# Kernel tuning notes

Measured on AMD Instinct MI355X. Metric: run time of the kernel, lower is better.

Reference implementation:

```python
import jax, jax.numpy as jnp
import numpy as np

NUM_INSTANCES = 64  # instance ids in [0, 64); id 0 is background and excluded


def _variance_smooth_loss(variances, ins_labels, num_segments):
    # variances: [N, D] float, ins_labels: [N] int
    N, D = variances.shape
    ones = jnp.ones((N,), dtype=variances.dtype)
    counts = jax.ops.segment_sum(ones, ins_labels, num_segments=num_segments)          # [S]
    sums = jax.ops.segment_sum(variances, ins_labels, num_segments=num_segments)       # [S, D]
    safe_counts = jnp.maximum(counts, 1.0)
    means = sums / safe_counts[:, None]                                                # per-instance mean [S, D]
    diff = variances - means[ins_labels]                                               # gather means back [N, D]
    sq = jnp.sum(diff * diff, axis=1)                                                  # [N]
    # per-instance MSE = sum of squared diffs / (K_i * D), matching nn.MSELoss (mean reduction)
    per_ins = jax.ops.segment_sum(sq, ins_labels, num_segments=num_segments) / (safe_counts * D)
    valid = (counts > 0) & (jnp.arange(num_segments) != 0)                             # skip id 0 & absent ids
    return jnp.sum(jnp.where(valid, per_ins, jnp.zeros_like(per_ins)))


def setup_inputs() -> dict:
    key = jax.random.key(0)
    k1, k2 = jax.random.split(key)
    N, D = 4_000_000, 8
    variances = jax.random.normal(k1, (N, D), dtype=jnp.float32)
    ins_labels = jax.random.randint(k2, (N,), 0, NUM_INSTANCES, dtype=jnp.int32)
    return {"variances": variances, "ins_labels": ins_labels}


def reference(variances, ins_labels):
    return _variance_smooth_loss(variances, ins_labels, NUM_INSTANCES)
```

## Files before the change

kernel.cpp:

```cpp
#include <hip/hip_runtime.h>

#define NUM_INST 64
#define BLOCK 256
#define GRID 3125
#define TILE_ROWS 256
#define SROW 9
#define PSTRIDE 1088
#define CHUNK 125

typedef __attribute__((ext_vector_type(8))) short bf16x8;
typedef __attribute__((ext_vector_type(4))) float f32x4;

__global__ __launch_bounds__(BLOCK) void vsl_main(const float4* __restrict__ rows,
                                                  const int* __restrict__ labels,
                                                  float* __restrict__ partial,
                                                  int n, int ntiles) {
    __shared__ float S[TILE_ROWS * SROW];
    __shared__ alignas(16) int Lab[TILE_ROWS];
    __shared__ float Cred[4][64];

    const int tid = threadIdx.x;
    const int w = tid >> 6;
    const int lane = tid & 63;
    const int g = lane >> 4;
    const int nn = lane & 15;
    const int f = nn & 7;
    const bool hi = nn >= 8;
    const int inst = 16 * w + nn;

    f32x4 acc = {0.f, 0.f, 0.f, 0.f};
    float cntf = 0.f;

    for (int tile = blockIdx.x; tile < ntiles; tile += GRID) {
        {
            const int r = 64 * w + lane;
            const int gr = tile * TILE_ROWS + r;
            const bool valid = gr < n;
            float4 a = make_float4(0, 0, 0, 0), b = make_float4(0, 0, 0, 0);
            int lb = 0;
            if (valid) { a = rows[2 * gr]; b = rows[2 * gr + 1]; lb = labels[gr]; }
            float* sp = &S[r * SROW];
            sp[0] = a.x; sp[1] = a.y; sp[2] = a.z; sp[3] = a.w;
            sp[4] = b.x; sp[5] = b.y; sp[6] = b.z; sp[7] = b.w;
            Lab[r] = lb;
            unsigned long long Md = __ballot(valid);
#pragma unroll
            for (int bp = 0; bp < 6; ++bp) {
                const unsigned long long bb = __ballot((lb >> bp) & 1);
                Md &= ((lane >> bp) & 1) ? bb : ~bb;
            }
            cntf += (float)__popcll(Md);
        }
        __syncthreads();

#pragma unroll
        for (int kb = 0; kb < 8; ++kb) {
            const int rb = kb * 32 + 8 * g;

            const float* bp0 = &S[rb * SROW + f];
            union { int i[4]; bf16x8 v; } bf;
#pragma unroll
            for (int jp = 0; jp < 4; ++jp) {
                float v0 = bp0[(2 * jp) * SROW];
                float v1 = bp0[(2 * jp + 1) * SROW];
                if (hi) { v0 *= v0; v1 *= v1; }
                const unsigned u0 = __float_as_uint(v0) + 0x8000u;
                const unsigned u1 = __float_as_uint(v1) + 0x8000u;
                bf.i[jp] = (int)__builtin_amdgcn_perm(u1, u0, 0x07060302u);
            }

            const int4 l0 = *(const int4*)&Lab[rb];
            const int4 l1 = *(const int4*)&Lab[rb + 4];
            union { int i[4]; bf16x8 v; } af;
            af.i[0] = ((l0.x == inst) ? 0x3F80 : 0) | ((l0.y == inst) ? 0x3F800000 : 0);
            af.i[1] = ((l0.z == inst) ? 0x3F80 : 0) | ((l0.w == inst) ? 0x3F800000 : 0);
            af.i[2] = ((l1.x == inst) ? 0x3F80 : 0) | ((l1.y == inst) ? 0x3F800000 : 0);
            af.i[3] = ((l1.z == inst) ? 0x3F80 : 0) | ((l1.w == inst) ? 0x3F800000 : 0);

            acc = __builtin_amdgcn_mfma_f32_16x16x32_bf16(af.v, bf.v, acc, 0, 0, 0);
        }
        __syncthreads();
    }

    Cred[w][lane] = cntf;
    __syncthreads();
    float* pb = &partial[(size_t)blockIdx.x * PSTRIDE];
#pragma unroll
    for (int r4 = 0; r4 < 4; ++r4) {
        const int instk = 16 * w + 4 * g + r4;
        pb[instk * 16 + nn] = acc[r4];
    }
    if (w == 0) {
        pb[1024 + lane] = Cred[0][lane] + Cred[1][lane] + Cred[2][lane] + Cred[3][lane];
    }
}

__global__ __launch_bounds__(BLOCK) void vsl_reduce(const float* __restrict__ partial,
                                                    float* __restrict__ gacc) {
    const int id = blockIdx.x * BLOCK + threadIdx.x;
    if (id >= 25 * PSTRIDE) return;
    const int chunk = id / PSTRIDE;
    const int j = id - chunk * PSTRIDE;
    float s = 0.f;
    const float* p = &partial[(size_t)chunk * CHUNK * PSTRIDE + j];
#pragma unroll 5
    for (int q = 0; q < CHUNK; ++q) s += p[(size_t)q * PSTRIDE];
    atomicAdd(&gacc[j], s);
}

__global__ __launch_bounds__(64) void vsl_final(const float* __restrict__ gacc,
                                                float* __restrict__ out) {
    const int i = threadIdx.x;
    float val = 0.f;
    const float cnt = gacc[1024 + i];
    if (i != 0 && cnt > 0.f) {
        const float* base = &gacc[i * 16];
        float ss = 0.f, m2 = 0.f;
#pragma unroll
        for (int d = 0; d < 8; ++d) {
            m2 += base[d] * base[d];
            ss += base[8 + d];
        }
        val = (ss - m2 / cnt) / (cnt * 8.0f);
    }
#pragma unroll
    for (int off = 32; off > 0; off >>= 1) val += __shfl_down(val, off, 64);
    if (i == 0) out[0] = val;
}

extern "C" void kernel_launch(void* const* d_in, const int* in_sizes, int n_in,
                              void* d_out, int out_size, void* d_ws, size_t ws_size,
                              hipStream_t stream) {
    const float* variances = (const float*)d_in[0];
    const int* labels = (const int*)d_in[1];
    const int n = in_sizes[1];
    const int ntiles = (n + TILE_ROWS - 1) / TILE_ROWS;

    float* gacc = (float*)d_ws;
    float* partial = (float*)((char*)d_ws + 8192);

    hipMemsetAsync(gacc, 0, PSTRIDE * sizeof(float), stream);
    vsl_main<<<GRID, BLOCK, 0, stream>>>((const float4*)variances, labels, partial, n, ntiles);
    vsl_reduce<<<(25 * PSTRIDE + BLOCK - 1) / BLOCK, BLOCK, 0, stream>>>(partial, gacc);
    vsl_final<<<1, 64, 0, stream>>>(gacc, (float*)d_out);
}
```

Measured before the change: 212.5 us.

## Pre-convert tiles to bf16 MFMA layout in LDS and prefetch next tile

Result: no change. 210.7 us (-0.9%).

```diff
diff --git a/kernel.cpp b/kernel.cpp
--- a/kernel.cpp
+++ b/kernel.cpp
@@ -4,7 +4,6 @@
 #define BLOCK 256
 #define GRID 3125
 #define TILE_ROWS 256
-#define SROW 9
 #define PSTRIDE 1088
 #define CHUNK 125
 
@@ -15,7 +14,7 @@
                                                   const int* __restrict__ labels,
                                                   float* __restrict__ partial,
                                                   int n, int ntiles) {
-    __shared__ float S[TILE_ROWS * SROW];
+    __shared__ alignas(16) short MT[8 * 16 * 4 * 8];
     __shared__ alignas(16) int Lab[TILE_ROWS];
     __shared__ float Cred[4][64];
 
@@ -24,51 +23,58 @@
     const int lane = tid & 63;
     const int g = lane >> 4;
     const int nn = lane & 15;
-    const int f = nn & 7;
-    const bool hi = nn >= 8;
     const int inst = 16 * w + nn;
+
+    const int r = tid;
+    const int wbase = ((r >> 5) * 512) + (((r >> 3) & 3) * 8) + (r & 7);
 
     f32x4 acc = {0.f, 0.f, 0.f, 0.f};
     float cntf = 0.f;
 
-    for (int tile = blockIdx.x; tile < ntiles; tile += GRID) {
-        {
-            const int r = 64 * w + lane;
-            const int gr = tile * TILE_ROWS + r;
-            const bool valid = gr < n;
-            float4 a = make_float4(0, 0, 0, 0), b = make_float4(0, 0, 0, 0);
-            int lb = 0;
-            if (valid) { a = rows[2 * gr]; b = rows[2 * gr + 1]; lb = labels[gr]; }
-            float* sp = &S[r * SROW];
-            sp[0] = a.x; sp[1] = a.y; sp[2] = a.z; sp[3] = a.w;
-            sp[4] = b.x; sp[5] = b.y; sp[6] = b.z; sp[7] = b.w;
-            Lab[r] = lb;
-            unsigned long long Md = __ballot(valid);
+    int tile = blockIdx.x;
+    bool pv = false;
+    float4 pa = make_float4(0, 0, 0, 0), pb = make_float4(0, 0, 0, 0);
+    int plb = 0;
+    if (tile < ntiles) {
+        const int gr = tile * TILE_ROWS + r;
+        pv = gr < n;
+        if (pv) { pa = rows[2 * gr]; pb = rows[2 * gr + 1]; plb = labels[gr]; }
+    }
+
+    while (tile < ntiles) {
+        unsigned long long Md = __ballot(pv);
 #pragma unroll
-            for (int bp = 0; bp < 6; ++bp) {
-                const unsigned long long bb = __ballot((lb >> bp) & 1);
-                Md &= ((lane >> bp) & 1) ? bb : ~bb;
-            }
-            cntf += (float)__popcll(Md);
+        for (int bp = 0; bp < 6; ++bp) {
+            const unsigned long long bb = __ballot((plb >> bp) & 1);
+            Md &= ((lane >> bp) & 1) ? bb : ~bb;
         }
+        cntf += (float)__popcll(Md);
+
+        float v[16];
+        v[0] = pa.x; v[1] = pa.y; v[2] = pa.z; v[3] = pa.w;
+        v[4] = pb.x; v[5] = pb.y; v[6] = pb.z; v[7] = pb.w;
+#pragma unroll
+        for (int c = 0; c < 8; ++c) v[8 + c] = v[c] * v[c];
+#pragma unroll
+        for (int c = 0; c < 16; ++c) {
+            const unsigned u = __float_as_uint(v[c]) + 0x8000u;
+            MT[wbase + c * 32] = (short)(u >> 16);
+        }
+        Lab[r] = plb;
         __syncthreads();
+
+        const int nt = tile + GRID;
+        pv = false; pa = make_float4(0, 0, 0, 0); pb = make_float4(0, 0, 0, 0); plb = 0;
+        if (nt < ntiles) {
+            const int gr = nt * TILE_ROWS + r;
+            pv = gr < n;
+            if (pv) { pa = rows[2 * gr]; pb = rows[2 * gr + 1]; plb = labels[gr]; }
+        }
 
 #pragma unroll
         for (int kb = 0; kb < 8; ++kb) {
             const int rb = kb * 32 + 8 * g;
-
-            const float* bp0 = &S[rb * SROW + f];
-            union { int i[4]; bf16x8 v; } bf;
-#pragma unroll
-            for (int jp = 0; jp < 4; ++jp) {
-                float v0 = bp0[(2 * jp) * SROW];
-                float v1 = bp0[(2 * jp + 1) * SROW];
-                if (hi) { v0 *= v0; v1 *= v1; }
-                const unsigned u0 = __float_as_uint(v0) + 0x8000u;
-                const unsigned u1 = __float_as_uint(v1) + 0x8000u;
-                bf.i[jp] = (int)__builtin_amdgcn_perm(u1, u0, 0x07060302u);
-            }
-
+            const bf16x8 bfrag = *(const bf16x8*)&MT[kb * 512 + nn * 32 + g * 8];
             const int4 l0 = *(const int4*)&Lab[rb];
             const int4 l1 = *(const int4*)&Lab[rb + 4];
             union { int i[4]; bf16x8 v; } af;
@@ -76,22 +82,22 @@
             af.i[1] = ((l0.z == inst) ? 0x3F80 : 0) | ((l0.w == inst) ? 0x3F800000 : 0);
             af.i[2] = ((l1.x == inst) ? 0x3F80 : 0) | ((l1.y == inst) ? 0x3F800000 : 0);
             af.i[3] = ((l1.z == inst) ? 0x3F80 : 0) | ((l1.w == inst) ? 0x3F800000 : 0);
-
-            acc = __builtin_amdgcn_mfma_f32_16x16x32_bf16(af.v, bf.v, acc, 0, 0, 0);
+            acc = __builtin_amdgcn_mfma_f32_16x16x32_bf16(af.v, bfrag, acc, 0, 0, 0);
         }
         __syncthreads();
+        tile = nt;
     }
 
     Cred[w][lane] = cntf;
     __syncthreads();
-    float* pb = &partial[(size_t)blockIdx.x * PSTRIDE];
+    float* pbk = &partial[(size_t)blockIdx.x * PSTRIDE];
 #pragma unroll
     for (int r4 = 0; r4 < 4; ++r4) {
         const int instk = 16 * w + 4 * g + r4;
-        pb[instk * 16 + nn] = acc[r4];
+        pbk[instk * 16 + nn] = acc[r4];
     }
     if (w == 0) {
-        pb[1024 + lane] = Cred[0][lane] + Cred[1][lane] + Cred[2][lane] + Cred[3][lane];
+        pbk[1024 + lane] = Cred[0][lane] + Cred[1][lane] + Cred[2][lane] + Cred[3][lane];
     }
 }
 
```
